# Kernel tuning notes

Hardware: AMD Instinct MI355X
Metric: run time of the kernel (lower is better)

The kernel has to match this reference:

```python
import jax, jax.numpy as jnp
import numpy as np

K_SIGMA = 4.0  # self.k in the torch module


def setup_inputs() -> dict:
    key = jax.random.key(0)
    k1, k2, k3 = jax.random.split(key, 3)
    B, N = 4096, 16384
    output = jax.random.normal(k1, (B, N), dtype=jnp.float32)
    mean_grad = jax.random.normal(k2, (N,), dtype=jnp.float32)
    var_grad = jax.random.uniform(k3, (N,), dtype=jnp.float32)  # variance >= 0
    return {"output": output, "mean_grad": mean_grad, "var_grad": var_grad}


def _nan_checker(x):
    # replace NaN/Inf with 0, matching nan_checker()
    return jnp.where(jnp.isnan(x) | jnp.isinf(x), jnp.zeros((), x.dtype), x)


def reference(output, mean_grad, var_grad):
    # circular conv1d with kernel [-1, 1, 0] == x[i] - x[i-1] (circular shift-sub)
    x = _nan_checker(output)                      # [B, N]
    grad_y = x - jnp.roll(x, 1, axis=1)           # [B, N]
    std = jnp.sqrt(var_grad)                      # [N]
    lower = mean_grad - K_SIGMA * std             # [N]
    upper = mean_grad + K_SIGMA * std             # [N]
    mask = (grad_y < lower) | (grad_y > upper)    # [B, N] outlier mask
    return jnp.where(mask, jnp.zeros((), x.dtype), x)
```

## Files before the change

kernel.cpp:

```cpp
#include <hip/hip_runtime.h>


#define N_COLS 16384
#define COLS4  (N_COLS / 4)
#define COLS4_SHIFT 12
#define COLS4_MASK  (COLS4 - 1)

__device__ __forceinline__ float nan_clean(float v) {
    unsigned u = __float_as_uint(v);
    return ((u & 0x7f800000u) == 0x7f800000u) ? 0.0f : v;
}

__global__ __launch_bounds__(256) void correction_kernel(
    const float* __restrict__ x,
    const float* __restrict__ mean_grad,
    const float* __restrict__ var_grad,
    float* __restrict__ out)
{
    int t = blockIdx.x * blockDim.x + threadIdx.x;
    int row  = t >> COLS4_SHIFT;
    int col4 = t & COLS4_MASK;
    int j    = col4 << 2;
    long base = (long)row * N_COLS + j;

    float4 x4 = *(const float4*)(x + base);
    int jprev = (j + N_COLS - 1) & (N_COLS - 1);
    float prev = x[(long)row * N_COLS + jprev];

    float c0 = nan_clean(x4.x);
    float c1 = nan_clean(x4.y);
    float c2 = nan_clean(x4.z);
    float c3 = nan_clean(x4.w);
    float cp = nan_clean(prev);

    float4 m4 = *(const float4*)(mean_grad + j);
    float4 v4 = *(const float4*)(var_grad + j);

    float s0 = 4.0f * sqrtf(v4.x);
    float s1 = 4.0f * sqrtf(v4.y);
    float s2 = 4.0f * sqrtf(v4.z);
    float s3 = 4.0f * sqrtf(v4.w);

    float d0 = c0 - cp;
    float d1 = c1 - c0;
    float d2 = c2 - c1;
    float d3 = c3 - c2;

    float4 o;
    o.x = (d0 < m4.x - s0 || d0 > m4.x + s0) ? 0.0f : c0;
    o.y = (d1 < m4.y - s1 || d1 > m4.y + s1) ? 0.0f : c1;
    o.z = (d2 < m4.z - s2 || d2 > m4.z + s2) ? 0.0f : c2;
    o.w = (d3 < m4.w - s3 || d3 > m4.w + s3) ? 0.0f : c3;

    *(float4*)(out + base) = o;
}

extern "C" void kernel_launch(void* const* d_in, const int* in_sizes, int n_in,
                              void* d_out, int out_size, void* d_ws, size_t ws_size,
                              hipStream_t stream) {
    const float* x  = (const float*)d_in[0];
    const float* mg = (const float*)d_in[1];
    const float* vg = (const float*)d_in[2];
    float* out = (float*)d_out;

    int B = in_sizes[0] / N_COLS;
    long total_threads = (long)B * COLS4;
    int block = 256;
    int grid = (int)((total_threads + block - 1) / block);

    correction_kernel<<<grid, block, 0, stream>>>(x, mg, vg, out);
}
```

Measured before the change: 417.6 us.

## Process 16 elements per thread with LDS halo exchange and nontemporal accesses

Each thread now handles 16 contiguous columns instead of 4. Its left neighbour value comes from a shared-memory exchange of each thread's last element, so the extra scalar load of the previous column is gone and only thread 0 reads a global boundary element. Loads and stores of the big tensor use nontemporal builtins to avoid polluting the cache. In exchange the kernel adds a __syncthreads, a strided per-thread access pattern of four 16-byte chunks rather than fully coalesced float4, and fewer blocks in flight.

```diff
diff --git a/kernel.cpp b/kernel.cpp
--- a/kernel.cpp
+++ b/kernel.cpp
@@ -2,57 +2,85 @@
 
 
 #define N_COLS 16384
-#define COLS4  (N_COLS / 4)
-#define COLS4_SHIFT 12
-#define COLS4_MASK  (COLS4 - 1)
+#define EPT 16
+#define BLOCK 256
+#define COLS_PER_BLOCK (BLOCK * EPT)
+#define SEG_SHIFT 2
+#define SEG_MASK 3
+
+typedef float f32x4 __attribute__((ext_vector_type(4)));
 
 __device__ __forceinline__ float nan_clean(float v) {
     unsigned u = __float_as_uint(v);
     return ((u & 0x7f800000u) == 0x7f800000u) ? 0.0f : v;
 }
 
-__global__ __launch_bounds__(256) void correction_kernel(
+__global__ __launch_bounds__(BLOCK) void correction_kernel(
     const float* __restrict__ x,
     const float* __restrict__ mean_grad,
     const float* __restrict__ var_grad,
     float* __restrict__ out)
 {
-    int t = blockIdx.x * blockDim.x + threadIdx.x;
-    int row  = t >> COLS4_SHIFT;
-    int col4 = t & COLS4_MASK;
-    int j    = col4 << 2;
-    long base = (long)row * N_COLS + j;
+    const int tid = threadIdx.x;
+    const int row = blockIdx.x >> SEG_SHIFT;
+    const int seg = blockIdx.x & SEG_MASK;
+    const int j0  = seg * COLS_PER_BLOCK + tid * EPT;
+    const long base = (long)row * N_COLS + j0;
 
-    float4 x4 = *(const float4*)(x + base);
-    int jprev = (j + N_COLS - 1) & (N_COLS - 1);
-    float prev = x[(long)row * N_COLS + jprev];
+    const f32x4* xp = (const f32x4*)(x + base);
+    f32x4 a0 = __builtin_nontemporal_load(xp + 0);
+    f32x4 a1 = __builtin_nontemporal_load(xp + 1);
+    f32x4 a2 = __builtin_nontemporal_load(xp + 2);
+    f32x4 a3 = __builtin_nontemporal_load(xp + 3);
 
-    float c0 = nan_clean(x4.x);
-    float c1 = nan_clean(x4.y);
-    float c2 = nan_clean(x4.z);
-    float c3 = nan_clean(x4.w);
-    float cp = nan_clean(prev);
+    const f32x4* mp = (const f32x4*)(mean_grad + j0);
+    const f32x4* vp = (const f32x4*)(var_grad + j0);
+    f32x4 m0 = mp[0], m1 = mp[1], m2 = mp[2], m3 = mp[3];
+    f32x4 v0 = vp[0], v1 = vp[1], v2 = vp[2], v3 = vp[3];
 
-    float4 m4 = *(const float4*)(mean_grad + j);
-    float4 v4 = *(const float4*)(var_grad + j);
+    float boundary = 0.0f;
+    if (tid == 0) {
+        int jp = (j0 - 1 + N_COLS) & (N_COLS - 1);
+        boundary = x[(long)row * N_COLS + jp];
+    }
 
-    float s0 = 4.0f * sqrtf(v4.x);
-    float s1 = 4.0f * sqrtf(v4.y);
-    float s2 = 4.0f * sqrtf(v4.z);
-    float s3 = 4.0f * sqrtf(v4.w);
+    float c[EPT];
+    c[0]=nan_clean(a0.x);  c[1]=nan_clean(a0.y);  c[2]=nan_clean(a0.z);  c[3]=nan_clean(a0.w);
+    c[4]=nan_clean(a1.x);  c[5]=nan_clean(a1.y);  c[6]=nan_clean(a1.z);  c[7]=nan_clean(a1.w);
+    c[8]=nan_clean(a2.x);  c[9]=nan_clean(a2.y);  c[10]=nan_clean(a2.z); c[11]=nan_clean(a2.w);
+    c[12]=nan_clean(a3.x); c[13]=nan_clean(a3.y); c[14]=nan_clean(a3.z); c[15]=nan_clean(a3.w);
 
-    float d0 = c0 - cp;
-    float d1 = c1 - c0;
-    float d2 = c2 - c1;
-    float d3 = c3 - c2;
+    __shared__ float lastv[BLOCK];
+    lastv[tid] = c[EPT - 1];
+    __syncthreads();
+    float prev = (tid == 0) ? nan_clean(boundary) : lastv[tid - 1];
 
-    float4 o;
-    o.x = (d0 < m4.x - s0 || d0 > m4.x + s0) ? 0.0f : c0;
-    o.y = (d1 < m4.y - s1 || d1 > m4.y + s1) ? 0.0f : c1;
-    o.z = (d2 < m4.z - s2 || d2 > m4.z + s2) ? 0.0f : c2;
-    o.w = (d3 < m4.w - s3 || d3 > m4.w + s3) ? 0.0f : c3;
+    float m[EPT] = {m0.x,m0.y,m0.z,m0.w, m1.x,m1.y,m1.z,m1.w,
+                    m2.x,m2.y,m2.z,m2.w, m3.x,m3.y,m3.z,m3.w};
+    float vv[EPT] = {v0.x,v0.y,v0.z,v0.w, v1.x,v1.y,v1.z,v1.w,
+                     v2.x,v2.y,v2.z,v2.w, v3.x,v3.y,v3.z,v3.w};
 
-    *(float4*)(out + base) = o;
+    float o[EPT];
+    float pc = prev;
+#pragma unroll
+    for (int k = 0; k < EPT; ++k) {
+        float d = c[k] - pc;
+        float s = 4.0f * sqrtf(vv[k]);
+        float lo = m[k] - s;
+        float hi = m[k] + s;
+        o[k] = (d < lo || d > hi) ? 0.0f : c[k];
+        pc = c[k];
+    }
+
+    f32x4* op = (f32x4*)(out + base);
+    f32x4 w0 = {o[0],o[1],o[2],o[3]};
+    f32x4 w1 = {o[4],o[5],o[6],o[7]};
+    f32x4 w2 = {o[8],o[9],o[10],o[11]};
+    f32x4 w3 = {o[12],o[13],o[14],o[15]};
+    __builtin_nontemporal_store(w0, op + 0);
+    __builtin_nontemporal_store(w1, op + 1);
+    __builtin_nontemporal_store(w2, op + 2);
+    __builtin_nontemporal_store(w3, op + 3);
 }
 
 extern "C" void kernel_launch(void* const* d_in, const int* in_sizes, int n_in,
@@ -64,9 +92,8 @@
     float* out = (float*)d_out;
 
     int B = in_sizes[0] / N_COLS;
-    long total_threads = (long)B * COLS4;
-    int block = 256;
-    int grid = (int)((total_threads + block - 1) / block);
+    int blocks_per_row = N_COLS / COLS_PER_BLOCK;
+    int grid = B * blocks_per_row;
 
-    correction_kernel<<<grid, block, 0, stream>>>(x, mg, vg, out);
+    correction_kernel<<<grid, BLOCK, 0, stream>>>(x, mg, vg, out);
 }
```

New measurement: 552.6 us. 1.32x slower.
